# Performance work log

Measured on AMD Instinct MI355X. Metric: run time of the kernel, lower is better.

The kernel has to match this reference:

```python
import jax, jax.numpy as jnp
import numpy as np

# dims: B=batch, S=seq len, H=heads, D=in_features per head, R=realizations, K=conv kernel
B, S, H, D, R, K = 2, 1024, 8, 64, 32, 128


def setup_inputs() -> dict:
    key = jax.random.key(0)
    kq, kk, kwq, kwk, kz = jax.random.split(key, 5)
    queries = jax.random.normal(kq, (B, S, H, D), jnp.float32)
    keys = jax.random.normal(kk, (B, S, H, D), jnp.float32)
    # depthwise conv weights, torch init: uniform[0,1), shape (C_out, 1, K) with groups=C_out
    wq = jax.random.uniform(kwq, (H * D, 1, K), jnp.float32)
    wk = jax.random.uniform(kwk, (H * D, 1, K), jnp.float32)
    # stochastic process noise z: (B*R, H*D, 4K+S), scaled by 1/sqrt(R*D)
    z = jax.random.normal(kz, (B * R, H * D, 4 * K + S), jnp.float32) / np.float32(np.sqrt(R * D))
    return {"queries": queries, "keys": keys, "wq": wq, "wk": wk, "z": z}


def _dwconv(x, w):
    # depthwise 1D cross-correlation, VALID padding (matches nn.Conv1d, groups=C)
    return jax.lax.conv_general_dilated(
        x, w, window_strides=(1,), padding='VALID',
        dimension_numbers=('NCH', 'OIH', 'NCH'),
        feature_group_count=w.shape[0])


def reference(queries, keys, wq, wk, z):
    # note the faithful swap from the source: kbar uses conv_q, qbar uses conv_k
    kbar = _dwconv(z, wq)[:, :, K:K + S].reshape(B, R, H, D, S)
    qbar = _dwconv(z, wk)[:, :, K:K + S].reshape(B, R, H, D, S)
    # fused broadcast-multiply + feature-dim reduction:
    # (qbar * queries[:,None]).sum(axis=3) then permute -> (B,S,H,R)
    qhat = jnp.einsum('brhds,bshd->bshr', qbar, queries)
    khat = jnp.einsum('brhds,bshd->bshr', kbar, keys)
    return qhat, khat
```

## Files before the change

kernel.cpp:

```cpp
#include <hip/hip_runtime.h>

#define BB 2
#define SS 1024
#define HH 8
#define DD 64
#define RR 32
#define KK 128
#define ZLEN 1536
#define HD 512

#define MS 256
#define DC 16
#define NTC 24
#define WROWS 192
#define WSEG (WROWS*DC)
#define PARTS_FLOATS (256*8*2*64*16)

typedef _Float16 f16x8 __attribute__((ext_vector_type(8)));
typedef _Float16 f16x2 __attribute__((ext_vector_type(2)));
typedef float    f32x16 __attribute__((ext_vector_type(16)));

__global__ __launch_bounds__(1024) void convspe_mfma(
    const float* __restrict__ q, const float* __restrict__ kmat,
    const float* __restrict__ wq, const float* __restrict__ wk,
    const float* __restrict__ z, float* __restrict__ parts)
{
    __shared__ __align__(16) _Float16 zbuf[4][16 * 32 * 16];
    __shared__ __align__(16) _Float16 wqs[WSEG];
    __shared__ __align__(16) _Float16 wks[WSEG];

    const int tid  = threadIdx.x;
    const int wv   = tid >> 6;
    const int ssub = __builtin_amdgcn_readfirstlane(wv & 7);
    const int half = __builtin_amdgcn_readfirstlane(wv >> 3);
    const int lane = tid & 63;
    const int rl   = lane & 31;
    const int hi   = lane >> 5;

    const int bx = blockIdx.x;
    const int dc = bx & 3, stile = (bx >> 2) & 3, h = (bx >> 4) & 7, b = bx >> 7;
    const int s0b = stile * MS;
    const int d0  = dc * DC;

    const int sr  = tid >> 5;
    const int sdp = (tid >> 2) & 7;
    const int sth = tid & 3;
    const float* zr0 = z + ((size_t)(b * RR + sr) * HD + h * DD + d0 + 2 * sdp) * ZLEN
                         + KK + s0b + sth * 4;
    const float* zr1 = zr0 + ZLEN;

    float4 ra0, rb0, ra1, rb1;
    auto loadch = [&](int tc, float4& a, float4& b) {
        a = *(const float4*)(zr0 + tc * 16);
        b = *(const float4*)(zr1 + tc * 16);
    };
    auto writech = [&](int tc, const float4& a, const float4& b) {
        f16x2* dst = (f16x2*)zbuf[tc & 3];
        const float av[4] = {a.x, a.y, a.z, a.w};
        const float bv[4] = {b.x, b.y, b.z, b.w};
        #pragma unroll
        for (int e = 0; e < 4; ++e) {
            const int ts = sth * 4 + e;
            dst[(ts * 32 + sr) * 8 + sdp] =
                __builtin_bit_cast(f16x2, __builtin_amdgcn_cvt_pkrtz(av[e], bv[e]));
        }
    };

    loadch(0, ra0, rb0);

    f16x8 qf, kf;
    {
        const int s = s0b + ssub * 32 + rl;
        const size_t base = (((size_t)b * SS + s) * HH + h) * DD + d0 + 8 * hi;
        #pragma unroll
        for (int j = 0; j < 8; ++j) {
            qf[j] = (_Float16)q[base + j];
            kf[j] = (_Float16)kmat[base + j];
        }
    }

    {
        const int t2 = tid & 511;
        const int di = t2 & 15, tq = t2 >> 4;
        const float* warr = (tid < 512) ? wq : wk;
        _Float16* wdst    = (tid < 512) ? wqs : wks;
        const float4 v4 = *(const float4*)&warr[(h * DD + dc * DC + di) * KK + tq * 4];
        const float av[4] = {v4.x, v4.y, v4.z, v4.w};
        #pragma unroll
        for (int e = 0; e < 4; ++e)
            wdst[(tq * 4 + e + 32) * 16 + di] = (_Float16)av[e];
        wdst[t2] = (_Float16)0.f;
        wdst[2560 + t2] = (_Float16)0.f;
    }

    f32x16 accq, acck;
    #pragma unroll
    for (int j = 0; j < 16; ++j) { accq[j] = 0.f; acck[j] = 0.f; }

    auto compute = [&](int tc) {
        const int tqbase = tc * 16 - ssub * 32;
        const int lo  = (tqbase < 0) ? -tqbase : 0;
        const int hi_ = (160 - tqbase < 16) ? (160 - tqbase) : 16;
        const int ps  = lo + ((lo ^ half) & 1);
        if (ps >= hi_) return;
        const _Float16* zb = zbuf[tc & 3];
        auto zrd = [&](int ts) {
            return *(const f16x8*)&zb[(ts * 32 + rl) * 16 + 8 * hi];
        };
        auto wrd = [&](const _Float16* ws, int ts) {
            const int row = tqbase + ts - rl + 32;
            return *(const f16x8*)&ws[row * 16 + 8 * hi];
        };
        f16x8 a0 = zrd(ps), k0 = wrd(wks, ps), q0 = wrd(wqs, ps);
        f16x8 a1 = a0, k1 = k0, q1 = q0;
        if (ps + 2 < hi_) { a1 = zrd(ps + 2); k1 = wrd(wks, ps + 2); q1 = wrd(wqs, ps + 2); }
        for (int ts = ps; ts < hi_ - 4; ts += 2) {
            const f16x8 a2 = zrd(ts + 4), k2 = wrd(wks, ts + 4), q2 = wrd(wqs, ts + 4);
            accq = __builtin_amdgcn_mfma_f32_32x32x16_f16(a0, k0 * qf, accq, 0, 0, 0);
            acck = __builtin_amdgcn_mfma_f32_32x32x16_f16(a0, q0 * kf, acck, 0, 0, 0);
            a0 = a1; k0 = k1; q0 = q1;
            a1 = a2; k1 = k2; q1 = q2;
        }
        accq = __builtin_amdgcn_mfma_f32_32x32x16_f16(a0, k0 * qf, accq, 0, 0, 0);
        acck = __builtin_amdgcn_mfma_f32_32x32x16_f16(a0, q0 * kf, acck, 0, 0, 0);
        if (ps + 2 < hi_) {
            accq = __builtin_amdgcn_mfma_f32_32x32x16_f16(a1, k1 * qf, accq, 0, 0, 0);
            acck = __builtin_amdgcn_mfma_f32_32x32x16_f16(a1, q1 * kf, acck, 0, 0, 0);
        }
    };

    loadch(1, ra1, rb1);
    writech(0, ra0, rb0);
    loadch(2, ra0, rb0);
    writech(1, ra1, rb1);
    loadch(3, ra1, rb1);
    __syncthreads();

    for (int t2 = 0; t2 < NTC; t2 += 2) {
        if (t2 + 2 < NTC) writech(t2 + 2, ra0, rb0);
        if (t2 + 4 < NTC) loadch(t2 + 4, ra0, rb0);
        compute(t2);
        if (t2 + 3 < NTC) writech(t2 + 3, ra1, rb1);
        if (t2 + 5 < NTC) loadch(t2 + 5, ra1, rb1);
        compute(t2 + 1);
        __syncthreads();
    }

    {
        float* mrg = (float*)zbuf;
        const int col = ssub * 64 + lane;
        if (half == 1) {
            #pragma unroll
            for (int j = 0; j < 16; ++j) mrg[j * 512 + col] = accq[j];
        }
        __syncthreads();
        if (half == 0) {
            #pragma unroll
            for (int j = 0; j < 16; ++j) accq[j] += mrg[j * 512 + col];
        }
        __syncthreads();
        if (half == 1) {
            #pragma unroll
            for (int j = 0; j < 16; ++j) mrg[j * 512 + col] = acck[j];
        }
        __syncthreads();
        if (half == 0) {
            #pragma unroll
            for (int j = 0; j < 16; ++j) acck[j] += mrg[j * 512 + col];
        }
    }

    if (half == 0) {
        float* pq = parts + ((((size_t)bx * 8 + ssub) * 2 + 0) * 64 + lane) * 16;
        float* pk = parts + ((((size_t)bx * 8 + ssub) * 2 + 1) * 64 + lane) * 16;
        #pragma unroll
        for (int g = 0; g < 4; ++g) {
            *(float4*)&pq[g * 4] = make_float4(accq[4*g], accq[4*g+1], accq[4*g+2], accq[4*g+3]);
            *(float4*)&pk[g * 4] = make_float4(acck[4*g], acck[4*g+1], acck[4*g+2], acck[4*g+3]);
        }
    }
}

__global__ __launch_bounds__(256) void reduce_kernel(
    const float* __restrict__ parts, float* __restrict__ out)
{
    const int idx = blockIdx.x * 256 + threadIdx.x;
    const int rq = idx & 7, h = (idx >> 3) & 7, s = (idx >> 6) & 1023;
    const int b = (idx >> 16) & 1, o = idx >> 17;
    const int stile = s >> 8, sub = (s >> 5) & 7, rl = s & 31;

    const int off = ((rq & 1) * 32 + rl) * 16 + 4 * (rq >> 1);

    float4 acc = make_float4(0.f, 0.f, 0.f, 0.f);
    #pragma unroll
    for (int dc = 0; dc < 4; ++dc) {
        const int bx = ((b * 8 + h) * 4 + stile) * 4 + dc;
        const float4 v = *(const float4*)&parts[(((size_t)bx * 8 + sub) * 2 + o) * 1024 + off];
        acc.x += v.x; acc.y += v.y; acc.z += v.z; acc.w += v.w;
    }
    *(float4*)&out[(size_t)idx * 4] = acc;
}

extern "C" void kernel_launch(void* const* d_in, const int* in_sizes, int n_in,
                              void* d_out, int out_size, void* d_ws, size_t ws_size,
                              hipStream_t stream) {
    const float* q  = (const float*)d_in[0];
    const float* k  = (const float*)d_in[1];
    const float* wq = (const float*)d_in[2];
    const float* wk = (const float*)d_in[3];
    const float* z  = (const float*)d_in[4];
    float* out = (float*)d_out;

    float* parts = (float*)d_ws;

    hipLaunchKernelGGL(convspe_mfma, dim3(256), dim3(1024), 0, stream,
                       q, k, wq, wk, z, parts);
    hipLaunchKernelGGL(reduce_kernel, dim3(1024), dim3(256), 0, stream, parts, out);
}
```

Measured before the change: 303.6 us.

## Remap blocks to XCDs and alternate chunk traversal direction for L2 reuse

After: 299.4 us. No clear change (-1.4%).

```diff
diff --git a/kernel.cpp b/kernel.cpp
--- a/kernel.cpp
+++ b/kernel.cpp
@@ -37,10 +37,18 @@
     const int rl   = lane & 31;
     const int hi   = lane >> 5;
 
-    const int bx = blockIdx.x;
-    const int dc = bx & 3, stile = (bx >> 2) & 3, h = (bx >> 4) & 7, b = bx >> 7;
-    const int s0b = stile * MS;
-    const int d0  = dc * DC;
+    const int bx   = blockIdx.x;
+    const int xcd  = bx & 7, slot = bx >> 3;
+    const int g    = xcd * 2 + (slot & 1);
+    const int i16  = slot >> 1;
+    const int b    = g >> 3, h = g & 7;
+    const int stile = i16 >> 2, dc = i16 & 3;
+    const int lbx  = ((b * 8 + h) * 4 + stile) * 4 + dc;
+    const int dir  = stile & 1;
+    const int s0b  = stile * MS;
+    const int d0   = dc * DC;
+
+    auto M = [&](int i) { return dir ? (NTC - 1 - i) : i; };
 
     const int sr  = tid >> 5;
     const int sdp = (tid >> 2) & 7;
@@ -50,14 +58,14 @@
     const float* zr1 = zr0 + ZLEN;
 
     float4 ra0, rb0, ra1, rb1;
-    auto loadch = [&](int tc, float4& a, float4& b) {
-        a = *(const float4*)(zr0 + tc * 16);
-        b = *(const float4*)(zr1 + tc * 16);
+    auto loadch = [&](int tc, float4& a, float4& b_) {
+        a  = *(const float4*)(zr0 + tc * 16);
+        b_ = *(const float4*)(zr1 + tc * 16);
     };
-    auto writech = [&](int tc, const float4& a, const float4& b) {
+    auto writech = [&](int tc, const float4& a, const float4& b_) {
         f16x2* dst = (f16x2*)zbuf[tc & 3];
         const float av[4] = {a.x, a.y, a.z, a.w};
-        const float bv[4] = {b.x, b.y, b.z, b.w};
+        const float bv[4] = {b_.x, b_.y, b_.z, b_.w};
         #pragma unroll
         for (int e = 0; e < 4; ++e) {
             const int ts = sth * 4 + e;
@@ -66,7 +74,7 @@
         }
     };
 
-    loadch(0, ra0, rb0);
+    loadch(M(0), ra0, rb0);
 
     f16x8 qf, kf;
     {
@@ -129,20 +137,20 @@
         }
     };
 
-    loadch(1, ra1, rb1);
-    writech(0, ra0, rb0);
-    loadch(2, ra0, rb0);
-    writech(1, ra1, rb1);
-    loadch(3, ra1, rb1);
+    loadch(M(1), ra1, rb1);
+    writech(M(0), ra0, rb0);
+    loadch(M(2), ra0, rb0);
+    writech(M(1), ra1, rb1);
+    loadch(M(3), ra1, rb1);
     __syncthreads();
 
-    for (int t2 = 0; t2 < NTC; t2 += 2) {
-        if (t2 + 2 < NTC) writech(t2 + 2, ra0, rb0);
-        if (t2 + 4 < NTC) loadch(t2 + 4, ra0, rb0);
-        compute(t2);
-        if (t2 + 3 < NTC) writech(t2 + 3, ra1, rb1);
-        if (t2 + 5 < NTC) loadch(t2 + 5, ra1, rb1);
-        compute(t2 + 1);
+    for (int i2 = 0; i2 < NTC; i2 += 2) {
+        if (i2 + 2 < NTC) writech(M(i2 + 2), ra0, rb0);
+        if (i2 + 4 < NTC) loadch(M(i2 + 4), ra0, rb0);
+        compute(M(i2));
+        if (i2 + 3 < NTC) writech(M(i2 + 3), ra1, rb1);
+        if (i2 + 5 < NTC) loadch(M(i2 + 5), ra1, rb1);
+        compute(M(i2 + 1));
         __syncthreads();
     }
 
@@ -171,12 +179,12 @@
     }
 
     if (half == 0) {
-        float* pq = parts + ((((size_t)bx * 8 + ssub) * 2 + 0) * 64 + lane) * 16;
-        float* pk = parts + ((((size_t)bx * 8 + ssub) * 2 + 1) * 64 + lane) * 16;
-        #pragma unroll
-        for (int g = 0; g < 4; ++g) {
-            *(float4*)&pq[g * 4] = make_float4(accq[4*g], accq[4*g+1], accq[4*g+2], accq[4*g+3]);
-            *(float4*)&pk[g * 4] = make_float4(acck[4*g], acck[4*g+1], acck[4*g+2], acck[4*g+3]);
+        float* pq = parts + ((((size_t)lbx * 8 + ssub) * 2 + 0) * 64 + lane) * 16;
+        float* pk = parts + ((((size_t)lbx * 8 + ssub) * 2 + 1) * 64 + lane) * 16;
+        #pragma unroll
+        for (int g2 = 0; g2 < 4; ++g2) {
+            *(float4*)&pq[g2 * 4] = make_float4(accq[4*g2], accq[4*g2+1], accq[4*g2+2], accq[4*g2+3]);
+            *(float4*)&pk[g2 * 4] = make_float4(acck[4*g2], acck[4*g2+1], acck[4*g2+2], acck[4*g2+3]);
         }
     }
 }
```
